# Kernel optimization log

Hardware: AMD Instinct MI355X
Metric: run time of the kernel (lower is better)

Reference implementation:

```python
import jax, jax.numpy as jnp
import numpy as np

REG = 0.1  # config['reg']


def _poly_filter(s, gammas):
    # Horner evaluation of sum_k gammas[k] * s**k (monomial basis, depth K=len-1).
    out = jnp.full_like(s, gammas[-1])
    for k in range(gammas.shape[0] - 2, -1, -1):
        out = out * s + gammas[k]
    return out


def setup_inputs() -> dict:
    key = jax.random.key(0)
    k1, k2, k3, k4, k5 = jax.random.split(key, 5)
    B, H, N, R = 4, 8, 4096, 64
    U = jax.random.normal(k1, (B, H, N, R), dtype=jnp.float32)
    Sigma = jax.random.normal(k2, (B, H, 1, R), dtype=jnp.float32)
    svd_V = jax.random.normal(k3, (B, H, N, R), dtype=jnp.float32)
    V = jax.random.normal(k4, (B, H, N, R), dtype=jnp.float32)
    mask = jnp.ones((B, N), dtype=jnp.float32)
    # learnable polynomial coefficients; gamma_0 fixed to 1 (fixI=True)
    gammas = jnp.concatenate([jnp.ones((1,), jnp.float32),
                              0.1 * jax.random.normal(k5, (4,), dtype=jnp.float32)])
    return {"U": U, "Sigma": Sigma, "svd_V": svd_V, "V": V, "mask": mask, "gammas": gammas}


def reference(U, Sigma, svd_V, V, mask, gammas):
    # Q: softmax over rank dim r
    Q = jax.nn.softmax(U, axis=-1)                                      # [B,H,N,r]
    # K: masked softmax over sequence dim N
    Kmat = jax.nn.softmax(svd_V - 1e9 * (1.0 - mask[:, None, :, None]), axis=-2)
    S = jax.nn.sigmoid(Sigma)                                           # [B,H,1,r]
    graph_filter = _poly_filter(S, gammas)                              # [B,H,1,r]
    # linear-attention ordering: (Q*filt) @ (K^T @ V), never forms NxN
    KtV = jnp.einsum('bhnr,bhnd->bhrd', Kmat, V)                        # [B,H,r,d]
    X = jnp.einsum('bhnr,bhrd->bhnd', Q * graph_filter, KtV)            # [B,H,N,d]
    r = Q.shape[-1]
    eye = jnp.eye(r, dtype=Q.dtype)
    symQ = jnp.einsum('bhnr,bhns->bhrs', Q, Q) - eye
    ortho_loss = REG * jnp.mean(jnp.abs(symQ), axis=(1, 2, 3))
    symK = jnp.einsum('bhnr,bhns->bhrs', Kmat, Kmat) - eye
    ortho_loss = ortho_loss + REG * jnp.mean(jnp.abs(symK), axis=(1, 2, 3))
    return X, ortho_loss
```

## Files before the change

### kernel.cpp

```cpp
#include <hip/hip_runtime.h>
#include <math.h>

#define NB 4
#define NH 8
#define BHN 32
#define SN 4096
#define RR 64
#define REGC 0.1f

#define MCH 32
#define MROWS 128
#define XCH 32
#define XROWS 128

typedef short s16x8 __attribute__((ext_vector_type(8)));
typedef float f32x4 __attribute__((ext_vector_type(4)));

__device__ __forceinline__ float wave_sum(float v) {
    #pragma unroll
    for (int off = 32; off; off >>= 1) v += __shfl_xor(v, off, 64);
    return v;
}
__device__ __forceinline__ float wave_sum64(float v) {
    v += __int_as_float(__builtin_amdgcn_update_dpp(0, __float_as_int(v), 0x121, 0xf, 0xf, true));
    v += __int_as_float(__builtin_amdgcn_update_dpp(0, __float_as_int(v), 0x122, 0xf, 0xf, true));
    v += __int_as_float(__builtin_amdgcn_update_dpp(0, __float_as_int(v), 0x124, 0xf, 0xf, true));
    v += __int_as_float(__builtin_amdgcn_update_dpp(0, __float_as_int(v), 0x128, 0xf, 0xf, true));
    v += __shfl_xor(v, 16, 64);
    v += __shfl_xor(v, 32, 64);
    return v;
}
__device__ __forceinline__ float octet_sum(float v) {
    v += __int_as_float(__builtin_amdgcn_update_dpp(0, __float_as_int(v), 0xB1, 0xf, 0xf, true));
    v += __int_as_float(__builtin_amdgcn_update_dpp(0, __float_as_int(v), 0x4E, 0xf, 0xf, true));
    v += __shfl_xor(v, 4, 64);
    return v;
}
__device__ __forceinline__ float fastrcp(float x) {
    float r; asm("v_rcp_f32 %0, %1" : "=v"(r) : "v"(x)); return r;
}
__device__ __forceinline__ unsigned short f2bf(float x) {
    unsigned int u = __float_as_uint(x);
    u += 0x7FFFu + ((u >> 16) & 1u);
    return (unsigned short)(u >> 16);
}
__device__ __forceinline__ float bf2f(unsigned short h) {
    return __uint_as_float(((unsigned int)h) << 16);
}
__device__ __forceinline__ unsigned int packbf(float a, float b) {
    return (unsigned int)f2bf(a) | ((unsigned int)f2bf(b) << 16);
}
__device__ __forceinline__ s16x8 ldfrag(const unsigned int* p) {
    uint4 r = *(const uint4*)p;
    return __builtin_bit_cast(s16x8, r);
}
__device__ __forceinline__ int swz(int row, int blk) {
    return (row << 5) + (((blk ^ (row & 7))) << 2);
}
__device__ __forceinline__ uint4 pack8(const float* x) {
    return make_uint4(packbf(x[0], x[1]), packbf(x[2], x[3]),
                      packbf(x[4], x[5]), packbf(x[6], x[7]));
}

#define PH 0
#define VH 2048
#define QH 4096
__launch_bounds__(512, 4)
__global__ void k_main(const float* __restrict__ U, const float* __restrict__ sv,
                       const float* __restrict__ V, const float* __restrict__ mask,
                       float* __restrict__ ktv_part, float* __restrict__ symk_part,
                       float* __restrict__ symq_part, float* __restrict__ colsum_part) {
    __shared__ __align__(16) unsigned int sm[6144];
    const int chunk = blockIdx.x, bh = blockIdx.y, b = bh >> 3;
    const int t = threadIdx.x, l = t & 63, w = t >> 6;
    const int r15 = l & 15, quad = l >> 4;
    const int ni = w & 3, mi0 = (w >> 2) << 1;
    const size_t rowbase = (size_t)bh * SN * RR;
    const int row0 = chunk * MROWS;

    float csum = 0.0f;
    f32x4 aKV[2], aSK[2], aSQ[2];
    #pragma unroll
    for (int j = 0; j < 2; j++) {
        aKV[j] = (f32x4){0.f, 0.f, 0.f, 0.f};
        aSK[j] = (f32x4){0.f, 0.f, 0.f, 0.f};
        aSQ[j] = (f32x4){0.f, 0.f, 0.f, 0.f};
    }

    float bu[2][8], bx[2][8], bv[2][8], bm[2][8];
    #pragma unroll
    for (int i = 0; i < 8; i++) {
        const size_t off = rowbase + (size_t)(row0 + 8 * w + i) * RR + l;
        bu[0][i] = U[off]; bx[0][i] = sv[off]; bv[0][i] = V[off];
        bm[0][i] = mask[b * SN + row0 + 8 * w + i];
    }

    #pragma unroll
    for (int s = 0; s < 2; s++) {
        const int cur = s & 1, nxt = cur ^ 1;
        const int nb = row0 + s * 64;
        if (s < 1) {
            #pragma unroll
            for (int i = 0; i < 8; i++) {
                const size_t off = rowbase + (size_t)(nb + 64 + 8 * w + i) * RR + l;
                bu[nxt][i] = U[off]; bx[nxt][i] = sv[off]; bv[nxt][i] = V[off];
                bm[nxt][i] = mask[b * SN + nb + 64 + 8 * w + i];
            }
        }
        float q[8], p[8];
        #pragma unroll
        for (int i = 0; i < 8; i++) {
            const float eu = __expf(bu[cur][i]);
            q[i] = eu * fastrcp(wave_sum64(eu));
        }
        #pragma unroll
        for (int i = 0; i < 8; i++) {
            p[i] = __expf(bx[cur][i] - 1e9f * (1.0f - bm[cur][i]));
            csum += p[i];
        }
        const uint4 ph = pack8(p);
        const uint4 vh = pack8(bv[cur]);
        const uint4 qh = pack8(q);
        const int wbase = (l << 5) + ((w ^ (l & 7)) << 2);
        if (s > 0) __syncthreads();
        *(uint4*)(sm + PH + wbase) = ph;
        *(uint4*)(sm + VH + wbase) = vh;
        *(uint4*)(sm + QH + wbase) = qh;
        __syncthreads();
        #pragma unroll
        for (int ks = 0; ks < 2; ks++) {
            const int ub = ks * 4 + quad;
            s16x8 Ah[2], AQ[2];
            #pragma unroll
            for (int j = 0; j < 2; j++) {
                const int oa = swz((mi0 + j) * 16 + r15, ub);
                Ah[j] = ldfrag(sm + PH + oa);
                AQ[j] = ldfrag(sm + QH + oa);
            }
            const int ob = swz(ni * 16 + r15, ub);
            const s16x8 Bvh = ldfrag(sm + VH + ob);
            const s16x8 Bph = ldfrag(sm + PH + ob);
            const s16x8 Bq  = ldfrag(sm + QH + ob);
            #pragma unroll
            for (int j = 0; j < 2; j++) {
                aKV[j] = __builtin_amdgcn_mfma_f32_16x16x32_bf16(Ah[j], Bvh, aKV[j], 0, 0, 0);
                aSK[j] = __builtin_amdgcn_mfma_f32_16x16x32_bf16(Ah[j], Bph, aSK[j], 0, 0, 0);
                aSQ[j] = __builtin_amdgcn_mfma_f32_16x16x32_bf16(AQ[j], Bq,  aSQ[j], 0, 0, 0);
            }
        }
    }
    const size_t pb = ((size_t)bh * MCH + chunk) * 4096;
    #pragma unroll
    for (int j = 0; j < 2; j++)
        #pragma unroll
        for (int r = 0; r < 4; r++) {
            const int e = ((mi0 + j) * 16 + quad * 4 + r) * 64 + ni * 16 + r15;
            ktv_part[pb + e]  = aKV[j][r];
            symk_part[pb + e] = aSK[j][r];
            symq_part[pb + e] = aSQ[j][r];
        }
    __syncthreads();
    float* smf = (float*)sm;
    smf[w * 64 + l] = csum;
    __syncthreads();
    if (w == 0) {
        float scol = 0.f;
        #pragma unroll
        for (int j = 0; j < 8; j++) scol += smf[j * 64 + l];
        colsum_part[(bh * MCH + chunk) * 64 + l] = scol;
    }
}

__global__ void k_finalize(const float* __restrict__ ktv_part, const float* __restrict__ symk_part,
                           const float* __restrict__ symq_part, const float* __restrict__ colsum_part,
                           const float* __restrict__ Sigma, const float* __restrict__ gammas,
                           unsigned short* __restrict__ ktvt_hi, unsigned short* __restrict__ ktvt_lo,
                           float* __restrict__ loss_part) {
    const int rb = blockIdx.x, bh = blockIdx.y, t = threadIdx.x;
    const int e = t & 127;
    const int h = t >> 7;
    const int idx = rb * 128 + e;
    float kv = 0.f, sk = 0.f, sq = 0.f;
    #pragma unroll
    for (int cc = 0; cc < 16; cc++) {
        const int ch = h * 16 + cc;
        const size_t pb = ((size_t)bh * MCH + ch) * 4096 + idx;
        kv += ktv_part[pb]; sk += symk_part[pb]; sq += symq_part[pb];
    }
    float csp = 0.f;
    if (t < 128) {
        const int col = t & 63, hc = t >> 6;
        #pragma unroll
        for (int cc = 0; cc < 16; cc++)
            csp += colsum_part[(bh * MCH + hc * 16 + cc) * 64 + col];
    }
    __shared__ float red[128][3];
    __shared__ float cs[64];
    __shared__ float smr[2];
    if (h == 1) { red[e][0] = kv; red[e][1] = sk; red[e][2] = sq; }
    if (t >= 64 && t < 128) cs[t - 64] = csp;
    __syncthreads();
    if (h == 0) { kv += red[e][0]; sk += red[e][1]; sq += red[e][2]; }
    if (t < 64) cs[t] += csp;
    __syncthreads();
    float lsum = 0.f;
    if (h == 0) {
        const int r = idx >> 6, c = idx & 63;
        const float iSr = fastrcp(cs[r]), iSc = fastrcp(cs[c]);
        const float g0 = gammas[0], g1 = gammas[1], g2 = gammas[2], g3 = gammas[3], g4 = gammas[4];
        const float sg = fastrcp(1.0f + __expf(-Sigma[bh * 64 + r]));
        float f = g4; f = f * sg + g3; f = f * sg + g2; f = f * sg + g1; f = f * sg + g0;
        const float kvf = kv * iSr * f;
        const unsigned short hi = f2bf(kvf);
        ktvt_hi[bh * 4096 + c * 64 + r] = hi;
        ktvt_lo[bh * 4096 + c * 64 + r] = f2bf(kvf - bf2f(hi));
        const float eye = (r == c) ? 1.0f : 0.0f;
        lsum = fabsf(sk * iSr * iSc - eye) + fabsf(sq - eye);
    }
    lsum = wave_sum(lsum);
    if ((t & 63) == 0 && t < 128) smr[t >> 6] = lsum;
    __syncthreads();
    if (t == 0) loss_part[bh * 32 + rb] = smr[0] + smr[1];
}

__launch_bounds__(512, 4)
__global__ void k_xq(const float* __restrict__ U,
                     const unsigned short* __restrict__ ktvt_hi,
                     const unsigned short* __restrict__ ktvt_lo,
                     const float* __restrict__ loss_part,
                     float* __restrict__ Xout, float* __restrict__ loss) {
    __shared__ __align__(16) unsigned int sm[4096];
    __shared__ float smr8[8];
    const int chunk = blockIdx.x, bh = blockIdx.y;
    const int t = threadIdx.x, l = t & 63, w = t >> 6;
    const int r15 = l & 15, quad = l >> 4;
    const int ni = w & 3, mi0 = (w >> 2) << 1;
    const size_t rowbase = (size_t)bh * SN * RR;
    const int row0 = chunk * XROWS;
    const int nl = 8 * w + (l >> 3);
    const int c0 = (l & 7) * 8;

    if (chunk == 0 && bh == 0) {
        float lv = loss_part[t * 2] + loss_part[t * 2 + 1];
        lv = wave_sum(lv);
        if ((t & 63) == 0) smr8[t >> 6] = lv;
    }

    s16x8 Bh[2], Bl[2];
    #pragma unroll
    for (int ks = 0; ks < 2; ks++) {
        const int idx = (ni * 16 + r15) * 64 + ks * 32 + quad * 8;
        Bh[ks] = __builtin_bit_cast(s16x8, *(const uint4*)(ktvt_hi + (size_t)bh * 4096 + idx));
        Bl[ks] = __builtin_bit_cast(s16x8, *(const uint4*)(ktvt_lo + (size_t)bh * 4096 + idx));
    }

    float4 ba[2], bb[2];
    {
        const float* src = U + rowbase + (size_t)(row0 + nl) * RR + c0;
        ba[0] = *(const float4*)src;
        bb[0] = *(const float4*)(src + 4);
    }

    #pragma unroll
    for (int s = 0; s < 2; s++) {
        const int cur = s & 1, nxt = cur ^ 1;
        const int nb = row0 + s * 64;
        const int bufb = cur * 2048;
        if (s < 1) {
            const float* src = U + rowbase + (size_t)(nb + 64 + nl) * RR + c0;
            ba[nxt] = *(const float4*)src;
            bb[nxt] = *(const float4*)(src + 4);
        }
        float e[8];
        e[0] = __expf(ba[cur].x); e[1] = __expf(ba[cur].y);
        e[2] = __expf(ba[cur].z); e[3] = __expf(ba[cur].w);
        e[4] = __expf(bb[cur].x); e[5] = __expf(bb[cur].y);
        e[6] = __expf(bb[cur].z); e[7] = __expf(bb[cur].w);
        float loc = 0.f;
        #pragma unroll
        for (int i = 0; i < 8; i++) loc += e[i];
        const float inv = fastrcp(octet_sum(loc));
        float q[8];
        #pragma unroll
        for (int i = 0; i < 8; i++) q[i] = e[i] * inv;
        *(uint4*)(sm + bufb + swz(nl, l & 7)) = pack8(q);
        __syncthreads();
        if (s == 0 && chunk == 0 && bh == 0 && t < 4)
            loss[t] = (REGC / (NH * 64.0f * 64.0f)) * (smr8[2 * t] + smr8[2 * t + 1]);
        f32x4 acc[2];
        acc[0] = (f32x4){0.f, 0.f, 0.f, 0.f};
        acc[1] = (f32x4){0.f, 0.f, 0.f, 0.f};
        #pragma unroll
        for (int ks = 0; ks < 2; ks++) {
            #pragma unroll
            for (int jj = 0; jj < 2; jj++) {
                const int oa = bufb + swz((mi0 + jj) * 16 + r15, ks * 4 + quad);
                const s16x8 Ah = ldfrag(sm + oa);
                acc[jj] = __builtin_amdgcn_mfma_f32_16x16x32_bf16(Ah, Bh[ks], acc[jj], 0, 0, 0);
                acc[jj] = __builtin_amdgcn_mfma_f32_16x16x32_bf16(Ah, Bl[ks], acc[jj], 0, 0, 0);
            }
        }
        #pragma unroll
        for (int jj = 0; jj < 2; jj++)
            #pragma unroll
            for (int r = 0; r < 4; r++) {
                const int n = nb + (mi0 + jj) * 16 + quad * 4 + r;
                __builtin_nontemporal_store(acc[jj][r],
                    &Xout[rowbase + (size_t)n * RR + ni * 16 + r15]);
            }
    }
}

extern "C" void kernel_launch(void* const* d_in, const int* in_sizes, int n_in,
                              void* d_out, int out_size, void* d_ws, size_t ws_size,
                              hipStream_t stream) {
    (void)in_sizes; (void)n_in; (void)out_size; (void)ws_size;
    const float* U      = (const float*)d_in[0];
    const float* Sigma  = (const float*)d_in[1];
    const float* sv     = (const float*)d_in[2];
    const float* V      = (const float*)d_in[3];
    const float* mask   = (const float*)d_in[4];
    const float* gammas = (const float*)d_in[5];

    float* X    = (float*)d_out;
    float* loss = X + (size_t)BHN * SN * RR;

    float* ws          = (float*)d_ws;
    float* ktv_part    = ws;
    float* symk_part   = ktv_part + (size_t)BHN * MCH * 4096;
    float* symq_part   = symk_part + (size_t)BHN * MCH * 4096;
    float* colsum_part = symq_part + (size_t)BHN * MCH * 4096;
    float* loss_part   = colsum_part + BHN * MCH * 64;
    unsigned short* ktvt_hi = (unsigned short*)(loss_part + 1024);
    unsigned short* ktvt_lo = ktvt_hi + BHN * 4096;

    hipLaunchKernelGGL(k_main, dim3(MCH, BHN), dim3(512), 0, stream,
                       U, sv, V, mask, ktv_part, symk_part, symq_part, colsum_part);
    hipLaunchKernelGGL(k_finalize, dim3(32, BHN), dim3(256), 0, stream,
                       ktv_part, symk_part, symq_part, colsum_part, Sigma, gammas,
                       ktvt_hi, ktvt_lo, loss_part);
    hipLaunchKernelGGL(k_xq, dim3(XCH, BHN), dim3(512), 0, stream,
                       U, ktvt_hi, ktvt_lo, loss_part, X, loss);
}
```

Baseline: 168.1 us.

## Double main-kernel rows per block, double-buffer LDS, use hardware bf16 pack and nontemporal loads

Each k_main block now processes 256 rows in four 64-row steps instead of 128 rows in two, which halves the number of partial results the finalize kernel must reduce. LDS is doubled so that consecutive steps use alternate buffers, removing the extra barrier before each store. The software round-to-nearest bf16 conversion is replaced with the v_cvt_pk_bf16_f32 instruction, and the streaming loads of U, svd_V and V are marked nontemporal. The costs are half as many main-kernel blocks, a larger LDS footprint that may lower occupancy, and a longer serial loop per block.

```diff
diff --git a/kernel.cpp b/kernel.cpp
--- a/kernel.cpp
+++ b/kernel.cpp
@@ -8,8 +8,8 @@
 #define RR 64
 #define REGC 0.1f
 
-#define MCH 32
-#define MROWS 128
+#define MCH 16
+#define MROWS 256
 #define XCH 32
 #define XROWS 128
 
@@ -47,8 +47,10 @@
 __device__ __forceinline__ float bf2f(unsigned short h) {
     return __uint_as_float(((unsigned int)h) << 16);
 }
-__device__ __forceinline__ unsigned int packbf(float a, float b) {
-    return (unsigned int)f2bf(a) | ((unsigned int)f2bf(b) << 16);
+__device__ __forceinline__ unsigned int pkbf(float lo, float hi) {
+    unsigned int r;
+    asm("v_cvt_pk_bf16_f32 %0, %1, %2" : "=v"(r) : "v"(lo), "v"(hi));
+    return r;
 }
 __device__ __forceinline__ s16x8 ldfrag(const unsigned int* p) {
     uint4 r = *(const uint4*)p;
@@ -58,8 +60,8 @@
     return (row << 5) + (((blk ^ (row & 7))) << 2);
 }
 __device__ __forceinline__ uint4 pack8(const float* x) {
-    return make_uint4(packbf(x[0], x[1]), packbf(x[2], x[3]),
-                      packbf(x[4], x[5]), packbf(x[6], x[7]));
+    return make_uint4(pkbf(x[0], x[1]), pkbf(x[2], x[3]),
+                      pkbf(x[4], x[5]), pkbf(x[6], x[7]));
 }
 
 #define PH 0
@@ -70,7 +72,7 @@
                        const float* __restrict__ V, const float* __restrict__ mask,
                        float* __restrict__ ktv_part, float* __restrict__ symk_part,
                        float* __restrict__ symq_part, float* __restrict__ colsum_part) {
-    __shared__ __align__(16) unsigned int sm[6144];
+    __shared__ __align__(16) unsigned int sm[12288];
     const int chunk = blockIdx.x, bh = blockIdx.y, b = bh >> 3;
     const int t = threadIdx.x, l = t & 63, w = t >> 6;
     const int r15 = l & 15, quad = l >> 4;
@@ -91,19 +93,24 @@
     #pragma unroll
     for (int i = 0; i < 8; i++) {
         const size_t off = rowbase + (size_t)(row0 + 8 * w + i) * RR + l;
-        bu[0][i] = U[off]; bx[0][i] = sv[off]; bv[0][i] = V[off];
+        bu[0][i] = __builtin_nontemporal_load(&U[off]);
+        bx[0][i] = __builtin_nontemporal_load(&sv[off]);
+        bv[0][i] = __builtin_nontemporal_load(&V[off]);
         bm[0][i] = mask[b * SN + row0 + 8 * w + i];
     }
 
     #pragma unroll
-    for (int s = 0; s < 2; s++) {
+    for (int s = 0; s < 4; s++) {
         const int cur = s & 1, nxt = cur ^ 1;
         const int nb = row0 + s * 64;
-        if (s < 1) {
+        const int bufb = cur * 6144;
+        if (s < 3) {
             #pragma unroll
             for (int i = 0; i < 8; i++) {
                 const size_t off = rowbase + (size_t)(nb + 64 + 8 * w + i) * RR + l;
-                bu[nxt][i] = U[off]; bx[nxt][i] = sv[off]; bv[nxt][i] = V[off];
+                bu[nxt][i] = __builtin_nontemporal_load(&U[off]);
+                bx[nxt][i] = __builtin_nontemporal_load(&sv[off]);
+                bv[nxt][i] = __builtin_nontemporal_load(&V[off]);
                 bm[nxt][i] = mask[b * SN + nb + 64 + 8 * w + i];
             }
         }
@@ -121,8 +128,7 @@
         const uint4 ph = pack8(p);
         const uint4 vh = pack8(bv[cur]);
         const uint4 qh = pack8(q);
-        const int wbase = (l << 5) + ((w ^ (l & 7)) << 2);
-        if (s > 0) __syncthreads();
+        const int wbase = bufb + (l << 5) + ((w ^ (l & 7)) << 2);
         *(uint4*)(sm + PH + wbase) = ph;
         *(uint4*)(sm + VH + wbase) = vh;
         *(uint4*)(sm + QH + wbase) = qh;
@@ -133,11 +139,11 @@
             s16x8 Ah[2], AQ[2];
             #pragma unroll
             for (int j = 0; j < 2; j++) {
-                const int oa = swz((mi0 + j) * 16 + r15, ub);
+                const int oa = bufb + swz((mi0 + j) * 16 + r15, ub);
                 Ah[j] = ldfrag(sm + PH + oa);
                 AQ[j] = ldfrag(sm + QH + oa);
             }
-            const int ob = swz(ni * 16 + r15, ub);
+            const int ob = bufb + swz(ni * 16 + r15, ub);
             const s16x8 Bvh = ldfrag(sm + VH + ob);
             const s16x8 Bph = ldfrag(sm + PH + ob);
             const s16x8 Bq  = ldfrag(sm + QH + ob);
@@ -182,8 +188,8 @@
     const int idx = rb * 128 + e;
     float kv = 0.f, sk = 0.f, sq = 0.f;
     #pragma unroll
-    for (int cc = 0; cc < 16; cc++) {
-        const int ch = h * 16 + cc;
+    for (int cc = 0; cc < 8; cc++) {
+        const int ch = h * 8 + cc;
         const size_t pb = ((size_t)bh * MCH + ch) * 4096 + idx;
         kv += ktv_part[pb]; sk += symk_part[pb]; sq += symq_part[pb];
     }
@@ -191,8 +197,8 @@
     if (t < 128) {
         const int col = t & 63, hc = t >> 6;
         #pragma unroll
-        for (int cc = 0; cc < 16; cc++)
-            csp += colsum_part[(bh * MCH + hc * 16 + cc) * 64 + col];
+        for (int cc = 0; cc < 8; cc++)
+            csp += colsum_part[(bh * MCH + hc * 8 + cc) * 64 + col];
     }
     __shared__ float red[128][3];
     __shared__ float cs[64];
@@ -280,10 +286,9 @@
         #pragma unroll
         for (int i = 0; i < 8; i++) loc += e[i];
         const float inv = fastrcp(octet_sum(loc));
-        float q[8];
-        #pragma unroll
-        for (int i = 0; i < 8; i++) q[i] = e[i] * inv;
-        *(uint4*)(sm + bufb + swz(nl, l & 7)) = pack8(q);
+        #pragma unroll
+        for (int i = 0; i < 8; i++) e[i] *= inv;
+        *(uint4*)(sm + bufb + swz(nl, l & 7)) = pack8(e);
         __syncthreads();
         if (s == 0 && chunk == 0 && bh == 0 && t < 4)
             loss[t] = (REGC / (NH * 64.0f * 64.0f)) * (smr8[2 * t] + smr8[2 * t + 1]);
```

Result: faster. 158.6 us (-5.7%).
